# Kernel tuning notes

Measured on AMD Instinct MI355X. Metric: run time of the kernel, lower is better.

The kernel has to match this reference:

```python
import jax, jax.numpy as jnp
import numpy as np

TEMPERATURE = 0.1  # init kwarg: temperature
A0 = 0.5           # init kwarg: a0 (scale on axis0 contrastive loss)
A1 = 0.5           # init kwarg: a1 (scale on axis1 contrastive loss)

N, D = 131072, 128     # examples, embedding dim
C, W = 8192, 8192      # unique csv ids, unique wiki ids


def setup_inputs() -> dict:
    key = jax.random.key(0)
    k1, k2, k3, k4 = jax.random.split(key, 4)
    f1 = jax.random.normal(k1, (N, D), dtype=jnp.float32)
    f2 = jax.random.normal(k2, (N, D), dtype=jnp.float32)
    csv_ids = jax.random.randint(k3, (N,), 0, C, dtype=jnp.int32)
    wiki_ids = jax.random.randint(k4, (N,), 0, W, dtype=jnp.int32)
    return {"f1": f1, "f2": f2, "csv_ids": csv_ids, "wiki_ids": wiki_ids,
            "num_csv": C, "num_wiki": W}


def _segment_mean(x, ids, n):
    # x: [N, D], ids: [N] in [0, n) -> [n, D] per-segment mean
    s = jax.ops.segment_sum(x, ids, num_segments=n)
    cnt = jax.ops.segment_sum(jnp.ones((x.shape[0],), x.dtype), ids, num_segments=n)
    return s / jnp.maximum(cnt, 1.0)[:, None]


def reference(f1, f2, csv_ids, wiki_ids, num_csv, num_wiki):
    # Segment-mean pooling (vectorized equivalent of the dict-of-lists loop).
    csv_emb = _segment_mean(f1, csv_ids, num_csv)    # [C, D]
    wiki_emb = _segment_mean(f2, wiki_ids, num_wiki)  # [W, D]

    # csv_wiki_map[row, col] = 1 for every observed (csv_id, wiki_id) pair.
    mask = jnp.zeros((num_csv, num_wiki), jnp.float32).at[csv_ids, wiki_ids].set(1.0)

    logits = jnp.matmul(csv_emb, wiki_emb.T) / TEMPERATURE  # [C, W]

    # log(exp(l)/sum_axis exp(l)) == log_softmax(l, axis) -- same math, stable/fused.
    lsm_ax1 = jax.nn.log_softmax(logits, axis=1)
    lsm_ax0 = jax.nn.log_softmax(logits, axis=0)

    row_cnt = jnp.maximum(jnp.sum(mask, axis=1), 1.0)
    col_cnt = jnp.maximum(jnp.sum(mask, axis=0), 1.0)

    axis1_loss = -jnp.mean(jnp.sum(lsm_ax1 * mask, axis=1) / row_cnt)
    axis0_loss = -jnp.mean(jnp.sum(lsm_ax0 * mask, axis=0) / col_cnt)

    return A0 * axis0_loss + A1 * axis1_loss
```

## Files before the change

kernel.cpp:

```cpp
#include <hip/hip_runtime.h>
#include <stdint.h>

#define N_EX 131072
#define DIM 128
#define NC 8192
#define NW 8192
#define LOG2E 1.4426950408889634f
#define LN2   0.6931471805599453f

typedef __attribute__((ext_vector_type(8))) __bf16 bf16x8;
typedef __attribute__((ext_vector_type(8))) unsigned short us8;
typedef __attribute__((ext_vector_type(4))) unsigned short us4;
typedef __attribute__((ext_vector_type(4))) float f32x4;

__device__ __forceinline__ unsigned short f2bf(float f) {
    union { float f; unsigned u; } v; v.f = f;
    unsigned u = v.u;
    unsigned r = u + 0x7fffu + ((u >> 16) & 1u);
    return (unsigned short)(r >> 16);
}
__device__ __forceinline__ float bf2f(unsigned lo16) {
    union { unsigned u; float f; } x; x.u = lo16 << 16; return x.f;
}
__device__ __forceinline__ float fexp2(float x) { return __builtin_amdgcn_exp2f(x); }
__device__ __forceinline__ float flog2(float x) { return __builtin_amdgcn_logf(x); }

template<int CTRL>
__device__ __forceinline__ float dpp_addf(float x) {
    int t = __builtin_amdgcn_update_dpp(0, __builtin_bit_cast(int, x), CTRL, 0xf, 0xf, true);
    return x + __builtin_bit_cast(float, t);
}
template<int CTRL>
__device__ __forceinline__ float dpp_maxf(float x) {
    int t = __builtin_amdgcn_update_dpp(0, __builtin_bit_cast(int, x), CTRL, 0xf, 0xf, true);
    return fmaxf(x, __builtin_bit_cast(float, t));
}
__device__ __forceinline__ float row16_sum(float s) {
    s = dpp_addf<0x128>(s); s = dpp_addf<0x124>(s);
    s = dpp_addf<0x122>(s); s = dpp_addf<0x121>(s);
    return s;
}
__device__ __forceinline__ float row16_max(float m) {
    m = dpp_maxf<0x128>(m); m = dpp_maxf<0x124>(m);
    m = dpp_maxf<0x122>(m); m = dpp_maxf<0x121>(m);
    return m;
}

__global__ void k_count(const int* __restrict__ cid, const int* __restrict__ wid,
                        int* cnt_c, int* cnt_w, unsigned* bitmask,
                        int* u_row, int* u_col, int* __restrict__ isuniq) {
    int i = blockIdx.x * blockDim.x + threadIdx.x;
    if (i >= N_EX) return;
    int c = cid[i], w = wid[i];
    atomicAdd(&cnt_c[c], 1);
    atomicAdd(&cnt_w[w], 1);
    unsigned key = ((unsigned)c << 13) | (unsigned)w;
    unsigned bit = 1u << (key & 31);
    unsigned old = atomicOr(&bitmask[key >> 5], bit);
    int win = (old & bit) ? 0 : 1;
    isuniq[i] = win;
    if (win) {
        atomicAdd(&u_row[c], 1);
        atomicAdd(&u_col[w], 1);
    }
}

__global__ void k_scan(const int* __restrict__ cnt_c, const int* __restrict__ cnt_w,
                       int* off_c, int* off_w, int* cur_c, int* cur_w) {
    const int* cnt = blockIdx.x ? cnt_w : cnt_c;
    int* offs = blockIdx.x ? off_w : off_c;
    int* cur  = blockIdx.x ? cur_w : cur_c;
    __shared__ int sh[1024];
    int t = threadIdx.x;
    int loc[8]; int s = 0;
#pragma unroll
    for (int j = 0; j < 8; j++) { loc[j] = s; s += cnt[t * 8 + j]; }
    sh[t] = s; __syncthreads();
    for (int o = 1; o < 1024; o <<= 1) {
        int v = (t >= o) ? sh[t - o] : 0;
        __syncthreads();
        sh[t] += v;
        __syncthreads();
    }
    int pre = t ? sh[t - 1] : 0;
#pragma unroll
    for (int j = 0; j < 8; j++) { int v = pre + loc[j]; offs[t * 8 + j] = v; cur[t * 8 + j] = v; }
}

__global__ void k_scatter(const int* __restrict__ cid, const int* __restrict__ wid,
                          int* cur_c, int* cur_w, int* rl_c, int* rl_w) {
    int i = blockIdx.x * blockDim.x + threadIdx.x;
    if (i < N_EX) {
        int c = cid[i]; int p = atomicAdd(&cur_c[c], 1); rl_c[p] = i;
    } else if (i < 2 * N_EX) {
        int j = i - N_EX; int w = wid[j]; int p = atomicAdd(&cur_w[w], 1); rl_w[p] = j;
    }
}

__global__ __launch_bounds__(256) void k_gather(const float* __restrict__ f1, const float* __restrict__ f2,
                         const int* __restrict__ off_c, const int* __restrict__ off_w,
                         const int* __restrict__ cnt_c, const int* __restrict__ cnt_w,
                         const int* __restrict__ rl_c, const int* __restrict__ rl_w,
                         unsigned short* emb_c, unsigned short* emb_w) {
    int tid = threadIdx.x;
    int seg = blockIdx.x * 8 + (tid >> 5);
    int l32 = tid & 31;
    const float* f = blockIdx.y ? f2 : f1;
    const int* off = blockIdx.y ? off_w : off_c;
    const int* cnt = blockIdx.y ? cnt_w : cnt_c;
    const int* rl  = blockIdx.y ? rl_w  : rl_c;
    unsigned short* emb = blockIdx.y ? emb_w : emb_c;
    int n = cnt[seg], o = off[seg];
    float4 a = make_float4(0.f, 0.f, 0.f, 0.f);
    int j = 0;
    for (; j + 8 <= n; j += 8) {
        int idx[8];
#pragma unroll
        for (int u = 0; u < 8; u++) idx[u] = rl[o + j + u];
        float4 v[8];
#pragma unroll
        for (int u = 0; u < 8; u++) v[u] = *((const float4*)(f + (long)idx[u] * DIM) + l32);
        float4 s0, s1;
        s0.x = (v[0].x + v[1].x) + (v[2].x + v[3].x);
        s0.y = (v[0].y + v[1].y) + (v[2].y + v[3].y);
        s0.z = (v[0].z + v[1].z) + (v[2].z + v[3].z);
        s0.w = (v[0].w + v[1].w) + (v[2].w + v[3].w);
        s1.x = (v[4].x + v[5].x) + (v[6].x + v[7].x);
        s1.y = (v[4].y + v[5].y) + (v[6].y + v[7].y);
        s1.z = (v[4].z + v[5].z) + (v[6].z + v[7].z);
        s1.w = (v[4].w + v[5].w) + (v[6].w + v[7].w);
        a.x += s0.x + s1.x; a.y += s0.y + s1.y;
        a.z += s0.z + s1.z; a.w += s0.w + s1.w;
    }
    for (; j < n; j++) {
        float4 v = *((const float4*)(f + (long)rl[o + j] * DIM) + l32);
        a.x += v.x; a.y += v.y; a.z += v.z; a.w += v.w;
    }
    int dn = n > 1 ? n : 1;
    float scale = (blockIdx.y ? 1.0f : 10.0f * LOG2E) / (float)dn;
    us4 hv = (us4){f2bf(a.x * scale), f2bf(a.y * scale), f2bf(a.z * scale), f2bf(a.w * scale)};
    *(us4*)(emb + (long)seg * DIM + l32 * 4) = hv;
}

__global__ __launch_bounds__(256) void k_gemm(const unsigned short* __restrict__ ea,
                                              const unsigned short* __restrict__ eb,
                                              float2* __restrict__ rowpart,
                                              float2* __restrict__ colpart) {
    __shared__ unsigned short smem[2 * 128 * 128];
    int tid = threadIdx.x;
    int lane = tid & 63, wv = tid >> 6;
    int q = lane >> 4, l15 = lane & 15;
    int rowq = wv & 1, colq = wv >> 1;

    {
        int sub = lane >> 4;
        int cph = lane & 15;
#pragma unroll
        for (int j = 0; j < 8; j++) {
            int rbase = wv * 32 + j * 4;
            int r = rbase + sub;
            int cl = (cph - r) & 15;
            const unsigned short* ga = ea + ((long)(blockIdx.x * 128 + r)) * DIM + cl * 8;
            const unsigned short* gb = eb + ((long)(blockIdx.y * 128 + r)) * DIM + cl * 8;
            unsigned short* la = smem + rbase * 128;
            unsigned short* lb = smem + 16384 + rbase * 128;
            __builtin_amdgcn_global_load_lds((const __attribute__((address_space(1))) unsigned int*)ga,
                                             (__attribute__((address_space(3))) unsigned int*)la, 16, 0, 0);
            __builtin_amdgcn_global_load_lds((const __attribute__((address_space(1))) unsigned int*)gb,
                                             (__attribute__((address_space(3))) unsigned int*)lb, 16, 0, 0);
        }
    }
    __syncthreads();

    const unsigned short* Abase = smem + (rowq * 64 + l15) * 128;
    const unsigned short* Bbase = smem + 16384 + (colq * 64 + l15) * 128;

    f32x4 acc[4][4];
#pragma unroll
    for (int tm = 0; tm < 4; tm++)
#pragma unroll
        for (int tn = 0; tn < 4; tn++) acc[tm][tn] = (f32x4){0.f, 0.f, 0.f, 0.f};

#pragma unroll
    for (int s = 0; s < 4; s++) {
        int ph = (s * 4 + q + l15) & 15;
        bf16x8 a[4], b[4];
#pragma unroll
        for (int t = 0; t < 4; t++) {
            a[t] = __builtin_bit_cast(bf16x8, *(const us8*)(Abase + t * 2048 + ph * 8));
            b[t] = __builtin_bit_cast(bf16x8, *(const us8*)(Bbase + t * 2048 + ph * 8));
        }
#pragma unroll
        for (int tm = 0; tm < 4; tm++)
#pragma unroll
            for (int tn = 0; tn < 4; tn++)
                acc[tm][tn] = __builtin_amdgcn_mfma_f32_16x16x32_bf16(a[tm], b[tn], acc[tm][tn], 0, 0, 0);
    }

    float m;
    {
        f32x4 mv = acc[0][0];
#pragma unroll
        for (int tm = 0; tm < 4; tm++)
#pragma unroll
            for (int tn = 0; tn < 4; tn++) {
                if (tm == 0 && tn == 0) continue;
#pragma unroll
                for (int r = 0; r < 4; r++) mv[r] = fmaxf(mv[r], acc[tm][tn][r]);
            }
        m = fmaxf(fmaxf(mv[0], mv[1]), fmaxf(mv[2], mv[3]));
        m = row16_max(m);
        m = fmaxf(m, __shfl_xor(m, 16));
        m = fmaxf(m, __shfl_xor(m, 32));
    }
#pragma unroll
    for (int tm = 0; tm < 4; tm++)
#pragma unroll
        for (int tn = 0; tn < 4; tn++)
#pragma unroll
            for (int r = 0; r < 4; r++) acc[tm][tn][r] = fexp2(acc[tm][tn][r] - m);

#pragma unroll
    for (int tm = 0; tm < 4; tm++)
#pragma unroll
        for (int r = 0; r < 4; r++) {
            float s = acc[tm][0][r] + acc[tm][1][r] + acc[tm][2][r] + acc[tm][3][r];
            s = row16_sum(s);
            if (l15 == 0) {
                int row = blockIdx.x * 128 + rowq * 64 + tm * 16 + q * 4 + r;
                rowpart[(long)row * 128 + blockIdx.y * 2 + colq] = make_float2(m, s);
            }
        }
#pragma unroll
    for (int tn = 0; tn < 4; tn++) {
        float s = 0.f;
#pragma unroll
        for (int tm = 0; tm < 4; tm++)
#pragma unroll
            for (int r = 0; r < 4; r++) s += acc[tm][tn][r];
        s += __shfl_xor(s, 16); s += __shfl_xor(s, 32);
        if (q == 0) {
            int col = blockIdx.y * 128 + colq * 64 + tn * 16 + l15;
            colpart[(long)col * 128 + blockIdx.x * 2 + rowq] = make_float2(m, s);
        }
    }
}

__global__ void k_combine(const float4* __restrict__ rowpart, const float4* __restrict__ colpart,
                          float* __restrict__ lse_row, float* __restrict__ lse_col) {
    int gtid = blockIdx.x * blockDim.x + threadIdx.x;
    int gw = gtid >> 6, lane = gtid & 63;
    int side = gw >> 13;
    int idx = gw & 8191;
    const float4* part = side ? colpart : rowpart;
    float4 v = part[(long)idx * 64 + lane];
    float m = fmaxf(v.x, v.z);
    float s = v.y * fexp2(v.x - m) + v.w * fexp2(v.z - m);
#pragma unroll
    for (int o = 1; o < 64; o <<= 1) {
        float om = __shfl_xor(m, o), os = __shfl_xor(s, o);
        float M = fmaxf(m, om);
        s = s * fexp2(m - M) + os * fexp2(om - M);
        m = M;
    }
    if (lane == 0) {
        float* dst = side ? lse_col : lse_row;
        dst[idx] = m + flog2(fmaxf(s, 1e-35f));
    }
}

__global__ __launch_bounds__(256) void k_pairs(const int* __restrict__ cid,
                                               const int* __restrict__ wid,
                                               const int* __restrict__ isuniq,
                                               const unsigned short* __restrict__ ea,
                                               const unsigned short* __restrict__ eb,
                                               const float* __restrict__ lse_row,
                                               const float* __restrict__ lse_col,
                                               const int* __restrict__ u_row,
                                               const int* __restrict__ u_col,
                                               float2* __restrict__ block_part) {
    int tid = threadIdx.x;
    int lane = tid & 63;
    int quarter = lane >> 4, l16 = lane & 15;
    int gwave = (blockIdx.x * 256 + tid) >> 6;
    float a0 = 0.f, a1 = 0.f;
#pragma unroll
    for (int base = gwave * 4; base < N_EX; base += 65536) {
        int p = base + quarter;
        int c = cid[p], w = wid[p];
        float flag = (float)isuniq[p];
        us8 av = *(const us8*)(ea + (long)c * DIM + l16 * 8);
        us8 bv = *(const us8*)(eb + (long)w * DIM + l16 * 8);
        float s = 0.f;
#pragma unroll
        for (int j = 0; j < 8; j++) s += bf2f((unsigned)av[j]) * bf2f((unsigned)bv[j]);
        s = row16_sum(s);
        if (l16 == 0) {
            a1 += flag * (s - lse_row[c]) * LN2 / fmaxf((float)u_row[c], 1.f);
            a0 += flag * (s - lse_col[w]) * LN2 / fmaxf((float)u_col[w], 1.f);
        }
    }
    a0 += __shfl_xor(a0, 16); a0 += __shfl_xor(a0, 32);
    a1 += __shfl_xor(a1, 16); a1 += __shfl_xor(a1, 32);
    __shared__ float2 shp[4];
    if (lane == 0) shp[tid >> 6] = make_float2(a0, a1);
    __syncthreads();
    if (tid == 0) {
        float2 t = shp[0];
        t.x += shp[1].x + shp[2].x + shp[3].x;
        t.y += shp[1].y + shp[2].y + shp[3].y;
        block_part[blockIdx.x] = t;
    }
}

__global__ void k_fin(const float2* __restrict__ block_part, float* __restrict__ out) {
    __shared__ float2 sh[256];
    int t = threadIdx.x;
    float x = 0.f, y = 0.f;
    for (int i = t; i < 4096; i += 256) { float2 v = block_part[i]; x += v.x; y += v.y; }
    sh[t] = make_float2(x, y); __syncthreads();
    for (int o = 128; o > 0; o >>= 1) {
        if (t < o) { sh[t].x += sh[t + o].x; sh[t].y += sh[t + o].y; }
        __syncthreads();
    }
    if (t == 0) {
        out[0] = -(sh[0].x + sh[0].y) * (0.5f / 8192.0f);
    }
}

extern "C" void kernel_launch(void* const* d_in, const int* in_sizes, int n_in,
                              void* d_out, int out_size, void* d_ws, size_t ws_size,
                              hipStream_t stream) {
    const float* f1 = (const float*)d_in[0];
    const float* f2 = (const float*)d_in[1];
    const int* cid  = (const int*)d_in[2];
    const int* wid  = (const int*)d_in[3];
    float* out = (float*)d_out;

    char* ws = (char*)d_ws;
    size_t off = 0;
    auto alloc = [&](size_t bytes) -> void* {
        void* p = ws + off;
        off += (bytes + 255) & ~(size_t)255;
        return p;
    };
    unsigned* bitmask = (unsigned*)alloc((size_t)NC * NW / 8);
    int* cnt_c = (int*)alloc(NC * 4);
    int* cnt_w = (int*)alloc(NW * 4);
    int* u_row = (int*)alloc(NC * 4);
    int* u_col = (int*)alloc(NW * 4);
    size_t zero_bytes = off;
    int* off_c = (int*)alloc(NC * 4);
    int* off_w = (int*)alloc(NW * 4);
    int* cur_c = (int*)alloc(NC * 4);
    int* cur_w = (int*)alloc(NW * 4);
    int* rl_c = (int*)alloc((size_t)N_EX * 4);
    int* rl_w = (int*)alloc((size_t)N_EX * 4);
    int* isuniq = (int*)alloc((size_t)N_EX * 4);
    unsigned short* emb_c = (unsigned short*)alloc((size_t)NC * DIM * 2);
    unsigned short* emb_w = (unsigned short*)alloc((size_t)NW * DIM * 2);
    float2* rowpart = (float2*)alloc((size_t)NC * 128 * sizeof(float2));
    float2* colpart = (float2*)alloc((size_t)NW * 128 * sizeof(float2));
    float* lse_row = (float*)alloc(NC * 4);
    float* lse_col = (float*)alloc(NW * 4);
    float2* block_part = (float2*)alloc(4096 * sizeof(float2));

    hipMemsetAsync(d_ws, 0, zero_bytes, stream);

    k_count<<<(N_EX + 255) / 256, 256, 0, stream>>>(cid, wid, cnt_c, cnt_w, bitmask,
                                                    u_row, u_col, isuniq);
    k_scan<<<2, 1024, 0, stream>>>(cnt_c, cnt_w, off_c, off_w, cur_c, cur_w);
    k_scatter<<<(2 * N_EX + 255) / 256, 256, 0, stream>>>(cid, wid, cur_c, cur_w, rl_c, rl_w);
    k_gather<<<dim3(NC / 8, 2), 256, 0, stream>>>(f1, f2, off_c, off_w, cnt_c, cnt_w,
                                                  rl_c, rl_w, emb_c, emb_w);
    k_gemm<<<dim3(NC / 128, NW / 128), 256, 0, stream>>>(emb_c, emb_w, rowpart, colpart);
    k_combine<<<(16384 * 64) / 256, 256, 0, stream>>>((const float4*)rowpart, (const float4*)colpart,
                                                      lse_row, lse_col);
    k_pairs<<<4096, 256, 0, stream>>>(cid, wid, isuniq, emb_c, emb_w,
                                      lse_row, lse_col, u_row, u_col, block_part);
    k_fin<<<1, 256, 0, stream>>>(block_part, out);
}
```

Baseline: 272.9 us.

## Make GEMM persistent with double-buffered B tiles and atomic-free scatter via ranks

Result: no change. 274.6 us (+0.6%).

```diff
diff --git a/kernel.cpp b/kernel.cpp
--- a/kernel.cpp
+++ b/kernel.cpp
@@ -48,12 +48,13 @@
 
 __global__ void k_count(const int* __restrict__ cid, const int* __restrict__ wid,
                         int* cnt_c, int* cnt_w, unsigned* bitmask,
-                        int* u_row, int* u_col, int* __restrict__ isuniq) {
+                        int* u_row, int* u_col, int* __restrict__ isuniq,
+                        int* __restrict__ rank_c, int* __restrict__ rank_w) {
     int i = blockIdx.x * blockDim.x + threadIdx.x;
     if (i >= N_EX) return;
     int c = cid[i], w = wid[i];
-    atomicAdd(&cnt_c[c], 1);
-    atomicAdd(&cnt_w[w], 1);
+    rank_c[i] = atomicAdd(&cnt_c[c], 1);
+    rank_w[i] = atomicAdd(&cnt_w[w], 1);
     unsigned key = ((unsigned)c << 13) | (unsigned)w;
     unsigned bit = 1u << (key & 31);
     unsigned old = atomicOr(&bitmask[key >> 5], bit);
@@ -66,10 +67,9 @@
 }
 
 __global__ void k_scan(const int* __restrict__ cnt_c, const int* __restrict__ cnt_w,
-                       int* off_c, int* off_w, int* cur_c, int* cur_w) {
+                       int* off_c, int* off_w) {
     const int* cnt = blockIdx.x ? cnt_w : cnt_c;
     int* offs = blockIdx.x ? off_w : off_c;
-    int* cur  = blockIdx.x ? cur_w : cur_c;
     __shared__ int sh[1024];
     int t = threadIdx.x;
     int loc[8]; int s = 0;
@@ -84,16 +84,19 @@
     }
     int pre = t ? sh[t - 1] : 0;
 #pragma unroll
-    for (int j = 0; j < 8; j++) { int v = pre + loc[j]; offs[t * 8 + j] = v; cur[t * 8 + j] = v; }
+    for (int j = 0; j < 8; j++) offs[t * 8 + j] = pre + loc[j];
 }
 
 __global__ void k_scatter(const int* __restrict__ cid, const int* __restrict__ wid,
-                          int* cur_c, int* cur_w, int* rl_c, int* rl_w) {
+                          const int* __restrict__ rank_c, const int* __restrict__ rank_w,
+                          const int* __restrict__ off_c, const int* __restrict__ off_w,
+                          int* rl_c, int* rl_w) {
     int i = blockIdx.x * blockDim.x + threadIdx.x;
     if (i < N_EX) {
-        int c = cid[i]; int p = atomicAdd(&cur_c[c], 1); rl_c[p] = i;
+        rl_c[off_c[cid[i]] + rank_c[i]] = i;
     } else if (i < 2 * N_EX) {
-        int j = i - N_EX; int w = wid[j]; int p = atomicAdd(&cur_w[w], 1); rl_w[p] = j;
+        int j = i - N_EX;
+        rl_w[off_w[wid[j]] + rank_w[j]] = j;
     }
 }
 
@@ -146,102 +149,121 @@
                                               const unsigned short* __restrict__ eb,
                                               float2* __restrict__ rowpart,
                                               float2* __restrict__ colpart) {
-    __shared__ unsigned short smem[2 * 128 * 128];
+    __shared__ unsigned short sA[16384];
+    __shared__ unsigned short sB[2][16384];
     int tid = threadIdx.x;
     int lane = tid & 63, wv = tid >> 6;
     int q = lane >> 4, l15 = lane & 15;
     int rowq = wv & 1, colq = wv >> 1;
-
-    {
-        int sub = lane >> 4;
-        int cph = lane & 15;
-#pragma unroll
-        for (int j = 0; j < 8; j++) {
-            int rbase = wv * 32 + j * 4;
-            int r = rbase + sub;
-            int cl = (cph - r) & 15;
-            const unsigned short* ga = ea + ((long)(blockIdx.x * 128 + r)) * DIM + cl * 8;
-            const unsigned short* gb = eb + ((long)(blockIdx.y * 128 + r)) * DIM + cl * 8;
-            unsigned short* la = smem + rbase * 128;
-            unsigned short* lb = smem + 16384 + rbase * 128;
-            __builtin_amdgcn_global_load_lds((const __attribute__((address_space(1))) unsigned int*)ga,
-                                             (__attribute__((address_space(3))) unsigned int*)la, 16, 0, 0);
-            __builtin_amdgcn_global_load_lds((const __attribute__((address_space(1))) unsigned int*)gb,
-                                             (__attribute__((address_space(3))) unsigned int*)lb, 16, 0, 0);
-        }
-    }
-    __syncthreads();
-
-    const unsigned short* Abase = smem + (rowq * 64 + l15) * 128;
-    const unsigned short* Bbase = smem + 16384 + (colq * 64 + l15) * 128;
-
-    f32x4 acc[4][4];
-#pragma unroll
-    for (int tm = 0; tm < 4; tm++)
-#pragma unroll
-        for (int tn = 0; tn < 4; tn++) acc[tm][tn] = (f32x4){0.f, 0.f, 0.f, 0.f};
-
-#pragma unroll
-    for (int s = 0; s < 4; s++) {
-        int ph = (s * 4 + q + l15) & 15;
-        bf16x8 a[4], b[4];
-#pragma unroll
-        for (int t = 0; t < 4; t++) {
-            a[t] = __builtin_bit_cast(bf16x8, *(const us8*)(Abase + t * 2048 + ph * 8));
-            b[t] = __builtin_bit_cast(bf16x8, *(const us8*)(Bbase + t * 2048 + ph * 8));
-        }
-#pragma unroll
-        for (int tm = 0; tm < 4; tm++)
-#pragma unroll
-            for (int tn = 0; tn < 4; tn++)
-                acc[tm][tn] = __builtin_amdgcn_mfma_f32_16x16x32_bf16(a[tm], b[tn], acc[tm][tn], 0, 0, 0);
-    }
-
-    float m;
-    {
-        f32x4 mv = acc[0][0];
-#pragma unroll
-        for (int tm = 0; tm < 4; tm++)
-#pragma unroll
-            for (int tn = 0; tn < 4; tn++) {
-                if (tm == 0 && tn == 0) continue;
-#pragma unroll
-                for (int r = 0; r < 4; r++) mv[r] = fmaxf(mv[r], acc[tm][tn][r]);
-            }
-        m = fmaxf(fmaxf(mv[0], mv[1]), fmaxf(mv[2], mv[3]));
-        m = row16_max(m);
-        m = fmaxf(m, __shfl_xor(m, 16));
-        m = fmaxf(m, __shfl_xor(m, 32));
-    }
-#pragma unroll
-    for (int tm = 0; tm < 4; tm++)
-#pragma unroll
-        for (int tn = 0; tn < 4; tn++)
-#pragma unroll
-            for (int r = 0; r < 4; r++) acc[tm][tn][r] = fexp2(acc[tm][tn][r] - m);
-
-#pragma unroll
-    for (int tm = 0; tm < 4; tm++)
-#pragma unroll
-        for (int r = 0; r < 4; r++) {
-            float s = acc[tm][0][r] + acc[tm][1][r] + acc[tm][2][r] + acc[tm][3][r];
-            s = row16_sum(s);
-            if (l15 == 0) {
-                int row = blockIdx.x * 128 + rowq * 64 + tm * 16 + q * 4 + r;
-                rowpart[(long)row * 128 + blockIdx.y * 2 + colq] = make_float2(m, s);
+    int sub = lane >> 4;
+    int cph = lane & 15;
+
+    int bx = blockIdx.x & 63;
+    int byb = blockIdx.x >> 6;
+
+#pragma unroll
+    for (int j = 0; j < 8; j++) {
+        int rbase = wv * 32 + j * 4;
+        int r = rbase + sub;
+        int cl = (cph - r) & 15;
+        const unsigned short* ga = ea + ((long)(bx * 128 + r)) * DIM + cl * 8;
+        const unsigned short* gb = eb + ((long)(byb * 128 + r)) * DIM + cl * 8;
+        __builtin_amdgcn_global_load_lds((const __attribute__((address_space(1))) unsigned int*)ga,
+                                         (__attribute__((address_space(3))) unsigned int*)(sA + rbase * 128), 16, 0, 0);
+        __builtin_amdgcn_global_load_lds((const __attribute__((address_space(1))) unsigned int*)gb,
+                                         (__attribute__((address_space(3))) unsigned int*)(sB[0] + rbase * 128), 16, 0, 0);
+    }
+
+    const unsigned short* Abase = sA + (rowq * 64 + l15) * 128;
+
+    for (int i = 0; i < 16; i++) {
+        int by = byb + (i << 2);
+        __syncthreads();
+
+        if (i < 15) {
+            int byn = by + 4;
+            unsigned short* dst = sB[(i + 1) & 1];
+#pragma unroll
+            for (int j = 0; j < 8; j++) {
+                int rbase = wv * 32 + j * 4;
+                int r = rbase + sub;
+                int cl = (cph - r) & 15;
+                const unsigned short* gb = eb + ((long)(byn * 128 + r)) * DIM + cl * 8;
+                __builtin_amdgcn_global_load_lds((const __attribute__((address_space(1))) unsigned int*)gb,
+                                                 (__attribute__((address_space(3))) unsigned int*)(dst + rbase * 128), 16, 0, 0);
             }
         }
-#pragma unroll
-    for (int tn = 0; tn < 4; tn++) {
-        float s = 0.f;
+
+        const unsigned short* Bbase = sB[i & 1] + (colq * 64 + l15) * 128;
+
+        f32x4 acc[4][4];
 #pragma unroll
         for (int tm = 0; tm < 4; tm++)
 #pragma unroll
-            for (int r = 0; r < 4; r++) s += acc[tm][tn][r];
-        s += __shfl_xor(s, 16); s += __shfl_xor(s, 32);
-        if (q == 0) {
-            int col = blockIdx.y * 128 + colq * 64 + tn * 16 + l15;
-            colpart[(long)col * 128 + blockIdx.x * 2 + rowq] = make_float2(m, s);
+            for (int tn = 0; tn < 4; tn++) acc[tm][tn] = (f32x4){0.f, 0.f, 0.f, 0.f};
+
+#pragma unroll
+        for (int s = 0; s < 4; s++) {
+            int ph = (s * 4 + q + l15) & 15;
+            bf16x8 a[4], b[4];
+#pragma unroll
+            for (int t = 0; t < 4; t++) {
+                a[t] = __builtin_bit_cast(bf16x8, *(const us8*)(Abase + t * 2048 + ph * 8));
+                b[t] = __builtin_bit_cast(bf16x8, *(const us8*)(Bbase + t * 2048 + ph * 8));
+            }
+#pragma unroll
+            for (int tm = 0; tm < 4; tm++)
+#pragma unroll
+                for (int tn = 0; tn < 4; tn++)
+                    acc[tm][tn] = __builtin_amdgcn_mfma_f32_16x16x32_bf16(a[tm], b[tn], acc[tm][tn], 0, 0, 0);
+        }
+
+        float m;
+        {
+            f32x4 mv = acc[0][0];
+#pragma unroll
+            for (int tm = 0; tm < 4; tm++)
+#pragma unroll
+                for (int tn = 0; tn < 4; tn++) {
+                    if (tm == 0 && tn == 0) continue;
+#pragma unroll
+                    for (int r = 0; r < 4; r++) mv[r] = fmaxf(mv[r], acc[tm][tn][r]);
+                }
+            m = fmaxf(fmaxf(mv[0], mv[1]), fmaxf(mv[2], mv[3]));
+            m = row16_max(m);
+            m = fmaxf(m, __shfl_xor(m, 16));
+            m = fmaxf(m, __shfl_xor(m, 32));
+        }
+#pragma unroll
+        for (int tm = 0; tm < 4; tm++)
+#pragma unroll
+            for (int tn = 0; tn < 4; tn++)
+#pragma unroll
+                for (int r = 0; r < 4; r++) acc[tm][tn][r] = fexp2(acc[tm][tn][r] - m);
+
+#pragma unroll
+        for (int tm = 0; tm < 4; tm++)
+#pragma unroll
+            for (int r = 0; r < 4; r++) {
+                float s = acc[tm][0][r] + acc[tm][1][r] + acc[tm][2][r] + acc[tm][3][r];
+                s = row16_sum(s);
+                if (l15 == 0) {
+                    int row = bx * 128 + rowq * 64 + tm * 16 + q * 4 + r;
+                    rowpart[(long)row * 128 + by * 2 + colq] = make_float2(m, s);
+                }
+            }
+#pragma unroll
+        for (int tn = 0; tn < 4; tn++) {
+            float s = 0.f;
+#pragma unroll
+            for (int tm = 0; tm < 4; tm++)
+#pragma unroll
+                for (int r = 0; r < 4; r++) s += acc[tm][tn][r];
+            s += __shfl_xor(s, 16); s += __shfl_xor(s, 32);
+            if (q == 0) {
+                int col = by * 128 + colq * 64 + tn * 16 + l15;
+                colpart[(long)col * 128 + bx * 2 + rowq] = make_float2(m, s);
+            }
         }
     }
 }
@@ -352,8 +374,8 @@
     size_t zero_bytes = off;
     int* off_c = (int*)alloc(NC * 4);
     int* off_w = (int*)alloc(NW * 4);
-    int* cur_c = (int*)alloc(NC * 4);
-    int* cur_w = (int*)alloc(NW * 4);
+    int* rank_c = (int*)alloc((size_t)N_EX * 4);
+    int* rank_w = (int*)alloc((size_t)N_EX * 4);
     int* rl_c = (int*)alloc((size_t)N_EX * 4);
     int* rl_w = (int*)alloc((size_t)N_EX * 4);
     int* isuniq = (int*)alloc((size_t)N_EX * 4);
@@ -368,12 +390,13 @@
     hipMemsetAsync(d_ws, 0, zero_bytes, stream);
 
     k_count<<<(N_EX + 255) / 256, 256, 0, stream>>>(cid, wid, cnt_c, cnt_w, bitmask,
-                                                    u_row, u_col, isuniq);
-    k_scan<<<2, 1024, 0, stream>>>(cnt_c, cnt_w, off_c, off_w, cur_c, cur_w);
-    k_scatter<<<(2 * N_EX + 255) / 256, 256, 0, stream>>>(cid, wid, cur_c, cur_w, rl_c, rl_w);
+                                                    u_row, u_col, isuniq, rank_c, rank_w);
+    k_scan<<<2, 1024, 0, stream>>>(cnt_c, cnt_w, off_c, off_w);
+    k_scatter<<<(2 * N_EX + 255) / 256, 256, 0, stream>>>(cid, wid, rank_c, rank_w,
+                                                          off_c, off_w, rl_c, rl_w);
     k_gather<<<dim3(NC / 8, 2), 256, 0, stream>>>(f1, f2, off_c, off_w, cnt_c, cnt_w,
                                                   rl_c, rl_w, emb_c, emb_w);
-    k_gemm<<<dim3(NC / 128, NW / 128), 256, 0, stream>>>(emb_c, emb_w, rowpart, colpart);
+    k_gemm<<<256, 256, 0, stream>>>(emb_c, emb_w, rowpart, colpart);
     k_combine<<<(16384 * 64) / 256, 256, 0, stream>>>((const float4*)rowpart, (const float4*)colpart,
                                                       lse_row, lse_col);
     k_pairs<<<4096, 256, 0, stream>>>(cid, wid, isuniq, emb_c, emb_w,
```
